# Optimization experiments

Hardware: AMD Instinct MI355X
Metric: run time of the kernel (lower is better)

## Reference

```python
import jax, jax.numpy as jnp
import numpy as np

NUM_HEADS = 4
C_IN = 80   # in_channels[0] (raw camera BEV channels)
C = 126     # in_channels[1]
D = C + 2   # 128, inner attention dim


def _conv(x, w, b=None):
    # NCHW conv, 3x3, SAME padding (padding=1)
    y = jax.lax.conv_general_dilated(x, w, (1, 1), 'SAME',
                                     dimension_numbers=('NCHW', 'OIHW', 'NCHW'))
    if b is not None:
        y = y + b[None, :, None, None]
    return y


def setup_inputs() -> dict:
    key = jax.random.key(0)
    ks = jax.random.split(key, 16)
    s = 0.02
    inp = {
        'lidar_bev': jax.random.normal(ks[0], (1, C, 64, 64), jnp.float32),
        'cam_bev': jax.random.normal(ks[1], (1, C_IN, 64, 64), jnp.float32),
        'cam_enc_w': jax.random.normal(ks[2], (C, C_IN, 3, 3), jnp.float32) * s,
        'cam_enc_b': jnp.zeros((C,), jnp.float32),
        'cam_v_w': jax.random.normal(ks[3], (D, C), jnp.float32) * s,
        'cam_qk_w': jax.random.normal(ks[4], (2 * D, C), jnp.float32) * s,
        'cam_proj_w': jax.random.normal(ks[5], (C, D), jnp.float32) * s,
        'cam_proj_b': jnp.zeros((C,), jnp.float32),
        'lidar_v_w': jax.random.normal(ks[6], (D, C), jnp.float32) * s,
        'lidar_qk_w': jax.random.normal(ks[7], (2 * D, C), jnp.float32) * s,
        'lidar_proj_w': jax.random.normal(ks[8], (C, D), jnp.float32) * s,
        'lidar_proj_b': jnp.zeros((C,), jnp.float32),
        'fuser_w': jax.random.normal(ks[9], (C, 4 * C, 3, 3), jnp.float32) * s,
    }
    return inp


def reference(lidar_bev, cam_bev, cam_enc_w, cam_enc_b, cam_v_w, cam_qk_w,
              cam_proj_w, cam_proj_b, lidar_v_w, lidar_qk_w, lidar_proj_w,
              lidar_proj_b, fuser_w):
    B, Cc, H, W = lidar_bev.shape
    N = H * W
    nh, hd = NUM_HEADS, D // NUM_HEADS
    scale = Cc ** (-0.5)  # in_channels[1] ** -0.5

    cam_enc = _conv(cam_bev, cam_enc_w, cam_enc_b)  # [B,C,H,W] (SCNET stand-in)

    cam_f = cam_enc.reshape(B, Cc, N).transpose(0, 2, 1)     # [B,N,C]
    lid_f = lidar_bev.reshape(B, Cc, N).transpose(0, 2, 1)    # [B,N,C]

    def heads(x):  # [B,N,D] -> [B,nh,N,hd]
        return x.reshape(B, N, nh, hd).transpose(0, 2, 1, 3)

    cam_v = heads(cam_f @ cam_v_w.T)
    lid_v = heads(lid_f @ lidar_v_w.T)

    def qk(x, w):  # -> (q, k) each [B,nh,N,hd]
        t = (x @ w.T).reshape(B, N, 2, nh, hd).transpose(2, 0, 3, 1, 4)
        return t[0], t[1]

    lid_q, lid_k = qk(lid_f, lidar_qk_w)
    cam_q, cam_k = qk(cam_f, cam_qk_w)

    def merge(o):  # [B,nh,N,hd] -> [B,N,D]
        return o.transpose(0, 2, 1, 3).reshape(B, N, D)

    def to_map(x):  # [B,N,C] -> [B,C,H,W]
        return x.reshape(B, H, W, Cc).transpose(0, 3, 1, 2)

    # lidar-driven attention, reused against two value tensors
    lid_attn = jax.nn.softmax(jnp.einsum('bhnd,bhmd->bhnm', lid_q, lid_k) * scale, axis=-1)
    cam_by_lid = to_map(merge(lid_attn @ cam_v) @ cam_proj_w.T + cam_proj_b)
    cam_bev_l = cam_enc + cam_by_lid
    lid_by_lid = to_map(merge(lid_attn @ lid_v) @ lidar_proj_w.T + lidar_proj_b)
    lidar_bev_l = lidar_bev + lid_by_lid

    # camera-driven attention (note: original code uses lidar_proj for BOTH outputs here)
    cam_attn = jax.nn.softmax(jnp.einsum('bhnd,bhmd->bhnm', cam_q, cam_k) * scale, axis=-1)
    cam_by_cam = to_map(merge(cam_attn @ cam_v) @ lidar_proj_w.T + lidar_proj_b)
    cam_bev_c = cam_enc + cam_by_cam
    lid_by_cam = to_map(merge(cam_attn @ lid_v) @ lidar_proj_w.T + lidar_proj_b)
    lidar_bev_c = lidar_bev + lid_by_cam

    fused_in = jnp.concatenate([cam_bev_c, cam_bev_l, lidar_bev_c, lidar_bev_l], axis=1)
    return _conv(fused_in, fuser_w)
```

## Files before the change

kernel.cpp:

```cpp
#include <hip/hip_runtime.h>
#include <hip/hip_bf16.h>

typedef unsigned short ushort_t;
using f32x4  = __attribute__((ext_vector_type(4))) float;
using f32x16 = __attribute__((ext_vector_type(16))) float;
using bf16x8 = __attribute__((ext_vector_type(8))) short;
typedef unsigned uint2v __attribute__((ext_vector_type(2)));

#define N_PIX 4096

static __device__ __forceinline__ unsigned short f2bf(float f) {
  unsigned int u = __builtin_bit_cast(unsigned int, f);
  u += 0x7FFFu + ((u >> 16) & 1u);
  return (unsigned short)(u >> 16);
}
static __device__ __forceinline__ float bf2f(unsigned int us) {
  return __builtin_bit_cast(float, us << 16);
}

typedef union {
  uint4 u4;
  unsigned u[4];
  unsigned long long q[2];
  bf16x8 v;
  unsigned short us[8];
} fragU;

#define LDS_U32(p) ((unsigned)(uintptr_t)((__attribute__((address_space(3))) void*)(p)))

__global__ __launch_bounds__(256) void zero_span_k(uint4* __restrict__ p, int n16) {
  int i = blockIdx.x * 256 + threadIdx.x;
  if (i < n16) p[i] = (uint4){0u, 0u, 0u, 0u};
}

__global__ __launch_bounds__(256) void pack_w_k(
    const float* __restrict__ cam_enc_w, const float* __restrict__ fuser_w,
    const float* __restrict__ lid_proj_w, const float* __restrict__ cam_proj_w,
    const float* __restrict__ lid_qk_w, const float* __restrict__ cam_qk_w,
    const float* __restrict__ cam_v_w, const float* __restrict__ lid_v_w,
    ushort_t* __restrict__ Wp_c, ushort_t* __restrict__ Wp_f,
    ushort_t* __restrict__ Wp_lid, ushort_t* __restrict__ Wp_cam,
    ushort_t* __restrict__ Wq) {
  const float QSCALE = 0.08908708063747479f * 1.4426950408889634f;
  int idx = blockIdx.x * 256 + threadIdx.x;
  if (idx < 110592) {
    int kk = idx / 12288, r = idx % 12288;
    int co = r / 96, ci = r % 96;
    float v = (co < 126 && ci < 80) ? cam_enc_w[(co * 80 + ci) * 9 + kk] : 0.f;
    Wp_c[idx] = f2bf(v);
  } else if (idx < 700416) {
    int j = idx - 110592;
    int kk = j / 65536, r = j % 65536;
    int co = r / 512, ci = r % 512;
    float v = (co < 126 && ci < 504) ? fuser_w[(co * 504 + ci) * 9 + kk] : 0.f;
    Wp_f[j] = f2bf(v);
  } else if (idx < 716800) {
    int j = idx - 700416;
    int co = j >> 7, k = j & 127;
    Wp_lid[j] = f2bf(co < 126 ? lid_proj_w[co * 128 + k] : 0.f);
  } else if (idx < 733184) {
    int j = idx - 716800;
    int co = j >> 7, k = j & 127;
    Wp_cam[j] = f2bf(co < 126 ? cam_proj_w[co * 128 + k] : 0.f);
  } else if (idx < 831488) {
    int j = idx - 733184;
    int t = j >> 14, r = j & 16383;
    int row = r >> 7, ci = r & 127;
    float v = 0.f;
    if (ci < 126) {
      if (t == 0)      v = lid_qk_w[row * 126 + ci] * QSCALE;
      else if (t == 1) v = lid_qk_w[(128 + row) * 126 + ci];
      else if (t == 2) v = cam_qk_w[row * 126 + ci] * QSCALE;
      else if (t == 3) v = cam_qk_w[(128 + row) * 126 + ci];
      else if (t == 4) v = cam_v_w[row * 126 + ci];
      else             v = lid_v_w[row * 126 + ci];
    }
    Wq[j] = f2bf(v);
  }
}

__global__ __launch_bounds__(256) void convert_in_k(
    const float* __restrict__ cam, const float* __restrict__ lidar,
    ushort_t* __restrict__ m, ushort_t* __restrict__ h,
    ushort_t* __restrict__ lidBF) {
  int idx = blockIdx.x * 256 + threadIdx.x;
  if (idx < 327680) {
    int ch = idx >> 12, n = idx & 4095;
    int y = n >> 6, x = n & 63;
    unsigned short b = f2bf(cam[idx]);
    m[ch * 4224 + (y + 1) * 64 + x] = b;
    h[ch * 4356 + (y + 1) * 66 + (x + 1)] = b;
  } else {
    int j = idx - 327680;
    if (j < 516096) lidBF[j] = f2bf(lidar[j]);
  }
}

__global__ __launch_bounds__(256) void conv_mfma_k(
    const ushort_t* __restrict__ Amain,
    const ushort_t* __restrict__ Ahalo,
    const ushort_t* __restrict__ Wp,
    ushort_t* __restrict__ parts,
    int CIp, int ksteps) {
  __shared__ __align__(16) ushort_t Abuf[2][2048];
  const int y   = blockIdx.x;
  const int kk  = blockIdx.y;
  const int ky  = kk / 3, kx = kk - ky * 3;
  const int tid = threadIdx.x;
  const int w   = tid >> 6, l = tid & 63;
  const int lane15 = l & 15, g = l >> 4;
  const int yy1 = y + ky;

  const int ci_l = w * 8 + (l >> 5) * 4 + ((l & 7) >> 1);
  const int m0   = ((l >> 3) & 3) * 16 + (l & 1) * 8;
  const ushort_t* src;
  size_t plane;
  if (kx == 1) { plane = 66 * 64; src = Amain + (size_t)ci_l * plane + yy1 * 64 + m0; }
  else         { plane = 66 * 66; src = Ahalo + (size_t)ci_l * plane + yy1 * 66 + m0 + kx; }

  const ushort_t* wbase = Wp + ((size_t)kk * 128 + w * 32 + lane15) * CIp + g * 8;
  const unsigned tr_base = LDS_U32(&Abuf[0][0]) + (unsigned)(g * 1024 + lane15 * 8);

  f32x4 acc[4][2];
  #pragma unroll
  for (int q = 0; q < 4; ++q) {
    acc[q][0] = (f32x4){0.f, 0.f, 0.f, 0.f};
    acc[q][1] = (f32x4){0.f, 0.f, 0.f, 0.f};
  }

  __builtin_amdgcn_global_load_lds(
      (const __attribute__((address_space(1))) unsigned*)src,
      (__attribute__((address_space(3))) unsigned*)(&Abuf[0][w * 512]), 16, 0, 0);
  __syncthreads();

  for (int s = 0; s < ksteps; ++s) {
    if (s + 1 < ksteps) {
      const ushort_t* srcn = src + (size_t)(s + 1) * 32 * plane;
      __builtin_amdgcn_global_load_lds(
          (const __attribute__((address_space(1))) unsigned*)srcn,
          (__attribute__((address_space(3))) unsigned*)(&Abuf[(s + 1) & 1][w * 512]), 16, 0, 0);
    }
    const ushort_t* wb = wbase + s * 32;
    fragU fb0, fb1;
    fb0.u4 = *(const uint4*)(wb);
    fb1.u4 = *(const uint4*)(wb + 16 * CIp);

    unsigned ta = tr_base + (unsigned)((s & 1) << 12);
    unsigned long long r00, r01, r10, r11, r20, r21, r30, r31;
    asm volatile("ds_read_b64_tr_b16 %0, %1 offset:0"   : "=v"(r00) : "v"(ta));
    asm volatile("ds_read_b64_tr_b16 %0, %1 offset:512" : "=v"(r01) : "v"(ta));
    asm volatile("ds_read_b64_tr_b16 %0, %1 offset:128" : "=v"(r10) : "v"(ta));
    asm volatile("ds_read_b64_tr_b16 %0, %1 offset:640" : "=v"(r11) : "v"(ta));
    asm volatile("ds_read_b64_tr_b16 %0, %1 offset:256" : "=v"(r20) : "v"(ta));
    asm volatile("ds_read_b64_tr_b16 %0, %1 offset:768" : "=v"(r21) : "v"(ta));
    asm volatile("ds_read_b64_tr_b16 %0, %1 offset:384" : "=v"(r30) : "v"(ta));
    asm volatile("ds_read_b64_tr_b16 %0, %1 offset:896" : "=v"(r31) : "v"(ta));
    asm volatile("s_waitcnt lgkmcnt(0)" ::: "memory");
    __builtin_amdgcn_sched_barrier(0);

    fragU fa;
    fa.q[0] = r00; fa.q[1] = r01;
    acc[0][0] = __builtin_amdgcn_mfma_f32_16x16x32_bf16(fa.v, fb0.v, acc[0][0], 0, 0, 0);
    acc[0][1] = __builtin_amdgcn_mfma_f32_16x16x32_bf16(fa.v, fb1.v, acc[0][1], 0, 0, 0);
    fa.q[0] = r10; fa.q[1] = r11;
    acc[1][0] = __builtin_amdgcn_mfma_f32_16x16x32_bf16(fa.v, fb0.v, acc[1][0], 0, 0, 0);
    acc[1][1] = __builtin_amdgcn_mfma_f32_16x16x32_bf16(fa.v, fb1.v, acc[1][1], 0, 0, 0);
    fa.q[0] = r20; fa.q[1] = r21;
    acc[2][0] = __builtin_amdgcn_mfma_f32_16x16x32_bf16(fa.v, fb0.v, acc[2][0], 0, 0, 0);
    acc[2][1] = __builtin_amdgcn_mfma_f32_16x16x32_bf16(fa.v, fb1.v, acc[2][1], 0, 0, 0);
    fa.q[0] = r30; fa.q[1] = r31;
    acc[3][0] = __builtin_amdgcn_mfma_f32_16x16x32_bf16(fa.v, fb0.v, acc[3][0], 0, 0, 0);
    acc[3][1] = __builtin_amdgcn_mfma_f32_16x16x32_bf16(fa.v, fb1.v, acc[3][1], 0, 0, 0);
    __syncthreads();
  }

  ushort_t* pout = parts + (size_t)kk * 524288 + (size_t)(w * 32 + lane15) * 4096
                 + y * 64 + g * 4;
  #pragma unroll
  for (int q = 0; q < 4; ++q) {
    ushort4 p0, p1;
    p0.x = f2bf(acc[q][0][0]); p0.y = f2bf(acc[q][0][1]);
    p0.z = f2bf(acc[q][0][2]); p0.w = f2bf(acc[q][0][3]);
    p1.x = f2bf(acc[q][1][0]); p1.y = f2bf(acc[q][1][1]);
    p1.z = f2bf(acc[q][1][2]); p1.w = f2bf(acc[q][1][3]);
    *(ushort4*)(pout + q * 16)             = p0;
    *(ushort4*)(pout + 16 * 4096 + q * 16) = p1;
  }
}

__global__ __launch_bounds__(256) void reduce9_k(
    const ushort_t* __restrict__ parts, float* __restrict__ out,
    ushort_t* __restrict__ outbf, const float* __restrict__ bias) {
  int n0 = (blockIdx.x * 256 + threadIdx.x) * 8;
  int co = blockIdx.y;
  size_t off = (size_t)co * 4096 + n0;
  float s[8] = {0, 0, 0, 0, 0, 0, 0, 0};
  #pragma unroll
  for (int kk = 0; kk < 9; ++kk) {
    uint4 v = *(const uint4*)(parts + (size_t)kk * 524288 + off);
    s[0] += bf2f(v.x & 0xffffu); s[1] += bf2f(v.x >> 16);
    s[2] += bf2f(v.y & 0xffffu); s[3] += bf2f(v.y >> 16);
    s[4] += bf2f(v.z & 0xffffu); s[5] += bf2f(v.z >> 16);
    s[6] += bf2f(v.w & 0xffffu); s[7] += bf2f(v.w >> 16);
  }
  float b = bias ? bias[co] : 0.f;
  #pragma unroll
  for (int i = 0; i < 8; ++i) s[i] += b;
  f32x4 o0 = {s[0], s[1], s[2], s[3]};
  f32x4 o1 = {s[4], s[5], s[6], s[7]};
  *(f32x4*)(out + off)     = o0;
  *(f32x4*)(out + off + 4) = o1;
  if (outbf) {
    ushort4 b0, b1;
    b0.x = f2bf(s[0]); b0.y = f2bf(s[1]); b0.z = f2bf(s[2]); b0.w = f2bf(s[3]);
    b1.x = f2bf(s[4]); b1.y = f2bf(s[5]); b1.z = f2bf(s[6]); b1.w = f2bf(s[7]);
    *(ushort4*)(outbf + off)     = b0;
    *(ushort4*)(outbf + off + 4) = b1;
  }
}

__global__ __launch_bounds__(256) void qkv_mfma_k(
    const ushort_t* __restrict__ lidBF, const ushort_t* __restrict__ camBF,
    const ushort_t* __restrict__ Wq,
    ushort_t* __restrict__ lidQK, ushort_t* __restrict__ camQK,
    ushort_t* __restrict__ camV, ushort_t* __restrict__ lidV) {
  __shared__ __align__(16) ushort_t Abuf[2][2048];
  const int y = blockIdx.x, t = blockIdx.y;
  const ushort_t* X = (t >= 2 && t <= 4) ? camBF : lidBF;
  const int tid = threadIdx.x;
  const int w = tid >> 6, l = tid & 63;
  const int lane15 = l & 15, g = l >> 4;
  const int ci_l = w * 8 + (l >> 5) * 4 + ((l & 7) >> 1);
  const int m0   = ((l >> 3) & 3) * 16 + (l & 1) * 8;
  const ushort_t* src = X + (size_t)ci_l * 4096 + y * 64 + m0;
  const ushort_t* wbase = Wq + (size_t)t * 16384 + (w * 32 + lane15) * 128 + g * 8;
  const unsigned tr_base = LDS_U32(&Abuf[0][0]) + (unsigned)(g * 1024 + lane15 * 8);

  f32x4 acc[4][2];
  #pragma unroll
  for (int q = 0; q < 4; ++q) {
    acc[q][0] = (f32x4){0.f, 0.f, 0.f, 0.f};
    acc[q][1] = (f32x4){0.f, 0.f, 0.f, 0.f};
  }

  __builtin_amdgcn_global_load_lds(
      (const __attribute__((address_space(1))) unsigned*)src,
      (__attribute__((address_space(3))) unsigned*)(&Abuf[0][w * 512]), 16, 0, 0);
  __syncthreads();

  for (int s = 0; s < 4; ++s) {
    if (s < 3) {
      const ushort_t* srcn = src + (size_t)(s + 1) * 32 * 4096;
      __builtin_amdgcn_global_load_lds(
          (const __attribute__((address_space(1))) unsigned*)srcn,
          (__attribute__((address_space(3))) unsigned*)(&Abuf[(s + 1) & 1][w * 512]), 16, 0, 0);
    }
    const ushort_t* wb = wbase + s * 32;
    fragU fb0, fb1;
    fb0.u4 = *(const uint4*)(wb);
    fb1.u4 = *(const uint4*)(wb + 16 * 128);

    unsigned ta = tr_base + (unsigned)((s & 1) << 12);
    unsigned long long r00, r01, r10, r11, r20, r21, r30, r31;
    asm volatile("ds_read_b64_tr_b16 %0, %1 offset:0"   : "=v"(r00) : "v"(ta));
    asm volatile("ds_read_b64_tr_b16 %0, %1 offset:512" : "=v"(r01) : "v"(ta));
    asm volatile("ds_read_b64_tr_b16 %0, %1 offset:128" : "=v"(r10) : "v"(ta));
    asm volatile("ds_read_b64_tr_b16 %0, %1 offset:640" : "=v"(r11) : "v"(ta));
    asm volatile("ds_read_b64_tr_b16 %0, %1 offset:256" : "=v"(r20) : "v"(ta));
    asm volatile("ds_read_b64_tr_b16 %0, %1 offset:768" : "=v"(r21) : "v"(ta));
    asm volatile("ds_read_b64_tr_b16 %0, %1 offset:384" : "=v"(r30) : "v"(ta));
    asm volatile("ds_read_b64_tr_b16 %0, %1 offset:896" : "=v"(r31) : "v"(ta));
    asm volatile("s_waitcnt lgkmcnt(0)" ::: "memory");
    __builtin_amdgcn_sched_barrier(0);

    fragU fa;
    fa.q[0] = r00; fa.q[1] = r01;
    acc[0][0] = __builtin_amdgcn_mfma_f32_16x16x32_bf16(fa.v, fb0.v, acc[0][0], 0, 0, 0);
    acc[0][1] = __builtin_amdgcn_mfma_f32_16x16x32_bf16(fa.v, fb1.v, acc[0][1], 0, 0, 0);
    fa.q[0] = r10; fa.q[1] = r11;
    acc[1][0] = __builtin_amdgcn_mfma_f32_16x16x32_bf16(fa.v, fb0.v, acc[1][0], 0, 0, 0);
    acc[1][1] = __builtin_amdgcn_mfma_f32_16x16x32_bf16(fa.v, fb1.v, acc[1][1], 0, 0, 0);
    fa.q[0] = r20; fa.q[1] = r21;
    acc[2][0] = __builtin_amdgcn_mfma_f32_16x16x32_bf16(fa.v, fb0.v, acc[2][0], 0, 0, 0);
    acc[2][1] = __builtin_amdgcn_mfma_f32_16x16x32_bf16(fa.v, fb1.v, acc[2][1], 0, 0, 0);
    fa.q[0] = r30; fa.q[1] = r31;
    acc[3][0] = __builtin_amdgcn_mfma_f32_16x16x32_bf16(fa.v, fb0.v, acc[3][0], 0, 0, 0);
    acc[3][1] = __builtin_amdgcn_mfma_f32_16x16x32_bf16(fa.v, fb1.v, acc[3][1], 0, 0, 0);
    __syncthreads();
  }

  if (t < 4) {
    ushort_t* dst = (t < 2) ? lidQK : camQK;
    const int colbase = (t & 1) * 128 + w * 32 + lane15;
    #pragma unroll
    for (int q = 0; q < 4; ++q)
      #pragma unroll
      for (int tt = 0; tt < 2; ++tt)
        #pragma unroll
        for (int r = 0; r < 4; ++r) {
          int n = y * 64 + q * 16 + g * 4 + r;
          dst[(size_t)n * 256 + colbase + tt * 16] = f2bf(acc[q][tt][r]);
        }
  } else {
    ushort_t* dst = (t == 4) ? camV : lidV;
    ushort_t* pout = dst + (size_t)(w * 32 + lane15) * 4096 + y * 64 + g * 4;
    #pragma unroll
    for (int q = 0; q < 4; ++q) {
      ushort4 p0, p1;
      p0.x = f2bf(acc[q][0][0]); p0.y = f2bf(acc[q][0][1]);
      p0.z = f2bf(acc[q][0][2]); p0.w = f2bf(acc[q][0][3]);
      p1.x = f2bf(acc[q][1][0]); p1.y = f2bf(acc[q][1][1]);
      p1.z = f2bf(acc[q][1][2]); p1.w = f2bf(acc[q][1][3]);
      *(ushort4*)(pout + q * 16)             = p0;
      *(ushort4*)(pout + 16 * 4096 + q * 16) = p1;
    }
  }
}

__global__ __launch_bounds__(256) void flash_attn_mfma(
    const ushort_t* __restrict__ lidQK, const ushort_t* __restrict__ camQK,
    const ushort_t* __restrict__ camV, const ushort_t* __restrict__ lidV,
    ushort_t* __restrict__ OP, float2* __restrict__ ML) {
  const int i0    = blockIdx.x * 128;
  const int h     = blockIdx.y;
  const int attn  = blockIdx.z >> 1;
  const int half  = blockIdx.z & 1;
  const int kbase = half * 2048;
  const ushort_t* QK = attn ? camQK : lidQK;

  __shared__ __align__(16) ushort_t Ks[2][64 * 40];
  __shared__ __align__(16) ushort_t Vt[2][64 * 72];

  const int tid = threadIdx.x;
  const int w = tid >> 6, l = tid & 63;
  const int q31 = l & 31, hi = l >> 5;
  const int q0w = i0 + w * 32;

  const int srow = tid >> 2, sc = tid & 3;
  const ushort_t* Kg = QK + (size_t)(kbase + srow) * 256 + 128 + h * 32 + sc * 8;
  const ushort_t* Vg = ((srow >> 5) ? lidV : camV)
                     + (size_t)(h * 32 + (srow & 31)) * N_PIX + kbase;

  fragU qf0, qf1;
  qf0.u4 = *(const uint4*)(QK + (size_t)(q0w + q31) * 256 + h * 32 + hi * 8);
  qf1.u4 = *(const uint4*)(QK + (size_t)(q0w + q31) * 256 + h * 32 + 16 + hi * 8);

  {
    uint4 k4 = *(const uint4*)Kg;
    uint4 va = *(const uint4*)(Vg + sc * 8);
    uint4 vb = *(const uint4*)(Vg + (sc + 4) * 8);
    *(uint4*)(&Ks[0][srow * 40 + sc * 8]) = k4;
    *(uint4*)(&Vt[0][srow * 72 + sc * 8]) = va;
    *(uint4*)(&Vt[0][srow * 72 + (sc + 4) * 8]) = vb;
  }
  __syncthreads();

  f32x16 Oc = (f32x16)0.f, Ol = (f32x16)0.f;
  float lrun = 0.f, mrun = -1e30f;

  for (int it = 0; it < 32; ++it) {
    const int cur = it & 1, nxt = cur ^ 1;
    const bool more = (it + 1) < 32;
    uint4 kn, van, vbn;
    if (more) {
      kn  = *(const uint4*)(Kg + (size_t)(it + 1) * 16384);
      van = *(const uint4*)(Vg + (it + 1) * 64 + sc * 8);
      vbn = *(const uint4*)(Vg + (it + 1) * 64 + (sc + 4) * 8);
    }

    const ushort_t* kb = &Ks[cur][0];
    fragU k00, k01, k10, k11;
    k00.u4 = *(const uint4*)(kb + q31 * 40 + hi * 8);
    k01.u4 = *(const uint4*)(kb + q31 * 40 + 16 + hi * 8);
    k10.u4 = *(const uint4*)(kb + (32 + q31) * 40 + hi * 8);
    k11.u4 = *(const uint4*)(kb + (32 + q31) * 40 + 16 + hi * 8);
    f32x16 S0, S1;
    __builtin_amdgcn_s_setprio(1);
    S0 = __builtin_amdgcn_mfma_f32_32x32x16_bf16(k00.v, qf0.v, (f32x16)0.f, 0, 0, 0);
    S0 = __builtin_amdgcn_mfma_f32_32x32x16_bf16(k01.v, qf1.v, S0, 0, 0, 0);
    S1 = __builtin_amdgcn_mfma_f32_32x32x16_bf16(k10.v, qf0.v, (f32x16)0.f, 0, 0, 0);
    S1 = __builtin_amdgcn_mfma_f32_32x32x16_bf16(k11.v, qf1.v, S1, 0, 0, 0);
    __builtin_amdgcn_s_setprio(0);

    float mx = S0[0];
    #pragma unroll
    for (int j = 1; j < 16; ++j) mx = fmaxf(mx, S0[j]);
    #pragma unroll
    for (int j = 0; j < 16; ++j) mx = fmaxf(mx, S1[j]);
    if (__any(mx > mrun + 6.f)) {
      float gm = mx;
      gm = fmaxf(gm, __shfl_xor(gm, 1));
      gm = fmaxf(gm, __shfl_xor(gm, 2));
      gm = fmaxf(gm, __shfl_xor(gm, 4));
      gm = fmaxf(gm, __shfl_xor(gm, 8));
      gm = fmaxf(gm, __shfl_xor(gm, 16));
      gm = fmaxf(gm, __shfl_xor(gm, 32));
      if (gm > mrun) {
        float corr = __builtin_amdgcn_exp2f(mrun - gm);
        Oc = Oc * corr;
        Ol = Ol * corr;
        lrun *= corr;
        mrun = gm;
      }
    }
    float ps = 0.f;
    #pragma unroll
    for (int j = 0; j < 16; ++j) {
      float p = __builtin_amdgcn_exp2f(S0[j] - mrun);
      S0[j] = p; ps += p;
    }
    #pragma unroll
    for (int j = 0; j < 16; ++j) {
      float p = __builtin_amdgcn_exp2f(S1[j] - mrun);
      S1[j] = p; ps += p;
    }
    ps += __shfl_xor(ps, 32);
    lrun += ps;

    fragU pa0, pa1, pa2, pa3;
    {
      unsigned a0, a1, b0, b1;
      asm("v_cvt_pk_bf16_f32 %0, %1, %2" : "=v"(a0) : "v"(S0[0]),  "v"(S0[1]));
      asm("v_cvt_pk_bf16_f32 %0, %1, %2" : "=v"(a1) : "v"(S0[2]),  "v"(S0[3]));
      asm("v_cvt_pk_bf16_f32 %0, %1, %2" : "=v"(b0) : "v"(S0[4]),  "v"(S0[5]));
      asm("v_cvt_pk_bf16_f32 %0, %1, %2" : "=v"(b1) : "v"(S0[6]),  "v"(S0[7]));
      uint2v r0 = __builtin_amdgcn_permlane32_swap(a0, b0, false, false);
      uint2v r1 = __builtin_amdgcn_permlane32_swap(a1, b1, false, false);
      pa0.u[0] = r0[0]; pa0.u[1] = r1[0]; pa0.u[2] = r0[1]; pa0.u[3] = r1[1];
      asm("v_cvt_pk_bf16_f32 %0, %1, %2" : "=v"(a0) : "v"(S0[8]),  "v"(S0[9]));
      asm("v_cvt_pk_bf16_f32 %0, %1, %2" : "=v"(a1) : "v"(S0[10]), "v"(S0[11]));
      asm("v_cvt_pk_bf16_f32 %0, %1, %2" : "=v"(b0) : "v"(S0[12]), "v"(S0[13]));
      asm("v_cvt_pk_bf16_f32 %0, %1, %2" : "=v"(b1) : "v"(S0[14]), "v"(S0[15]));
      r0 = __builtin_amdgcn_permlane32_swap(a0, b0, false, false);
      r1 = __builtin_amdgcn_permlane32_swap(a1, b1, false, false);
      pa1.u[0] = r0[0]; pa1.u[1] = r1[0]; pa1.u[2] = r0[1]; pa1.u[3] = r1[1];
      asm("v_cvt_pk_bf16_f32 %0, %1, %2" : "=v"(a0) : "v"(S1[0]),  "v"(S1[1]));
      asm("v_cvt_pk_bf16_f32 %0, %1, %2" : "=v"(a1) : "v"(S1[2]),  "v"(S1[3]));
      asm("v_cvt_pk_bf16_f32 %0, %1, %2" : "=v"(b0) : "v"(S1[4]),  "v"(S1[5]));
      asm("v_cvt_pk_bf16_f32 %0, %1, %2" : "=v"(b1) : "v"(S1[6]),  "v"(S1[7]));
      r0 = __builtin_amdgcn_permlane32_swap(a0, b0, false, false);
      r1 = __builtin_amdgcn_permlane32_swap(a1, b1, false, false);
      pa2.u[0] = r0[0]; pa2.u[1] = r1[0]; pa2.u[2] = r0[1]; pa2.u[3] = r1[1];
      asm("v_cvt_pk_bf16_f32 %0, %1, %2" : "=v"(a0) : "v"(S1[8]),  "v"(S1[9]));
      asm("v_cvt_pk_bf16_f32 %0, %1, %2" : "=v"(a1) : "v"(S1[10]), "v"(S1[11]));
      asm("v_cvt_pk_bf16_f32 %0, %1, %2" : "=v"(b0) : "v"(S1[12]), "v"(S1[13]));
      asm("v_cvt_pk_bf16_f32 %0, %1, %2" : "=v"(b1) : "v"(S1[14]), "v"(S1[15]));
      r0 = __builtin_amdgcn_permlane32_swap(a0, b0, false, false);
      r1 = __builtin_amdgcn_permlane32_swap(a1, b1, false, false);
      pa3.u[0] = r0[0]; pa3.u[1] = r1[0]; pa3.u[2] = r0[1]; pa3.u[3] = r1[1];
    }

    const ushort_t* vb = &Vt[cur][0];
    __builtin_amdgcn_s_setprio(1);
    {
      fragU vc, vl;
      vc.u4 = *(const uint4*)(vb + q31 * 72 + hi * 8);
      vl.u4 = *(const uint4*)(vb + (32 + q31) * 72 + hi * 8);
      Oc = __builtin_amdgcn_mfma_f32_32x32x16_bf16(pa0.v, vc.v, Oc, 0, 0, 0);
      Ol = __builtin_amdgcn_mfma_f32_32x32x16_bf16(pa0.v, vl.v, Ol, 0, 0, 0);
      vc.u4 = *(const uint4*)(vb + q31 * 72 + 16 + hi * 8);
      vl.u4 = *(const uint4*)(vb + (32 + q31) * 72 + 16 + hi * 8);
      Oc = __builtin_amdgcn_mfma_f32_32x32x16_bf16(pa1.v, vc.v, Oc, 0, 0, 0);
      Ol = __builtin_amdgcn_mfma_f32_32x32x16_bf16(pa1.v, vl.v, Ol, 0, 0, 0);
      vc.u4 = *(const uint4*)(vb + q31 * 72 + 32 + hi * 8);
      vl.u4 = *(const uint4*)(vb + (32 + q31) * 72 + 32 + hi * 8);
      Oc = __builtin_amdgcn_mfma_f32_32x32x16_bf16(pa2.v, vc.v, Oc, 0, 0, 0);
      Ol = __builtin_amdgcn_mfma_f32_32x32x16_bf16(pa2.v, vl.v, Ol, 0, 0, 0);
      vc.u4 = *(const uint4*)(vb + q31 * 72 + 48 + hi * 8);
      vl.u4 = *(const uint4*)(vb + (32 + q31) * 72 + 48 + hi * 8);
      Oc = __builtin_amdgcn_mfma_f32_32x32x16_bf16(pa3.v, vc.v, Oc, 0, 0, 0);
      Ol = __builtin_amdgcn_mfma_f32_32x32x16_bf16(pa3.v, vl.v, Ol, 0, 0, 0);
    }
    __builtin_amdgcn_s_setprio(0);

    if (more) {
      *(uint4*)(&Ks[nxt][srow * 40 + sc * 8]) = kn;
      *(uint4*)(&Vt[nxt][srow * 72 + sc * 8]) = van;
      *(uint4*)(&Vt[nxt][srow * 72 + (sc + 4) * 8]) = vbn;
    }
    __syncthreads();
  }

  ushort_t* OPc = OP + (size_t)((attn * 2 + half) * 2 + 0) * 4096 * 128;
  ushort_t* OPl = OP + (size_t)((attn * 2 + half) * 2 + 1) * 4096 * 128;
  const int d = h * 32 + q31;
  #pragma unroll
  for (int reg = 0; reg < 16; ++reg) {
    int n = q0w + (reg & 3) + 8 * (reg >> 2) + 4 * hi;
    OPc[(size_t)n * 128 + d] = f2bf(Oc[reg]);
    OPl[(size_t)n * 128 + d] = f2bf(Ol[reg]);
  }
  if (l < 32) {
    float2 v; v.x = mrun; v.y = lrun;
    ML[(size_t)(attn * 2 + half) * 4096 + q0w + l] = v;
  }
}

__global__ __launch_bounds__(256) void proj_mfma_k(
    const ushort_t* __restrict__ OP, const float2* __restrict__ ML,
    const ushort_t* __restrict__ Wlid, const ushort_t* __restrict__ Wcam,
    const float* __restrict__ cam_enc, const float* __restrict__ lidar_bev,
    const float* __restrict__ cam_proj_b, const float* __restrict__ lid_proj_b,
    ushort_t* __restrict__ fm, ushort_t* __restrict__ fh) {
  const int n0 = blockIdx.x * 64;
  const int ot = blockIdx.y;
  const int attn = (ot == 0 || ot == 2) ? 1 : 0;
  const int vt = ot >> 1;
  const int tid = threadIdx.x;
  const int w = tid >> 6, l = tid & 63;
  const int m = l & 15, g = l >> 4;

  const ushort_t* Oa = OP + (size_t)((attn * 2 + 0) * 2 + vt) * 4096 * 128;
  const ushort_t* Ob = OP + (size_t)((attn * 2 + 1) * 2 + vt) * 4096 * 128;
  const float2* MLa = ML + (size_t)(attn * 2 + 0) * 4096;
  const float2* MLb = ML + (size_t)(attn * 2 + 1) * 4096;

  const int arow = n0 + w * 16 + m;
  float2 mla = MLa[arow], mlb = MLb[arow];
  float M  = fmaxf(mla.x, mlb.x);
  float wa = __builtin_amdgcn_exp2f(mla.x - M);
  float wb = __builtin_amdgcn_exp2f(mlb.x - M);
  float dn = wa * mla.y + wb * mlb.y;
  float aa = wa / dn, ab = wb / dn;

  fragU afr[4];
  #pragma unroll
  for (int s = 0; s < 4; ++s) {
    fragU xa, xb;
    xa.u4 = *(const uint4*)(Oa + (size_t)arow * 128 + s * 32 + g * 8);
    xb.u4 = *(const uint4*)(Ob + (size_t)arow * 128 + s * 32 + g * 8);
    #pragma unroll
    for (int j = 0; j < 8; ++j)
      afr[s].us[j] = f2bf(aa * bf2f(xa.us[j]) + ab * bf2f(xb.us[j]));
  }

  const ushort_t* W = (ot == 1) ? Wcam : Wlid;
  f32x4 acc[8];
  #pragma unroll
  for (int t = 0; t < 8; ++t) acc[t] = (f32x4){0.f, 0.f, 0.f, 0.f};
  #pragma unroll
  for (int s = 0; s < 4; ++s) {
    #pragma unroll
    for (int t = 0; t < 8; ++t) {
      fragU bfr;
      bfr.u4 = *(const uint4*)(W + (size_t)(t * 16 + m) * 128 + s * 32 + g * 8);
      acc[t] = __builtin_amdgcn_mfma_f32_16x16x32_bf16(afr[s].v, bfr.v, acc[t], 0, 0, 0);
    }
  }

  const float* res  = (ot < 2) ? cam_enc : lidar_bev;
  const float* bias = (ot == 1) ? cam_proj_b : lid_proj_b;
  const int doff = ot * 126;
  #pragma unroll
  for (int t = 0; t < 8; ++t) {
    int co = t * 16 + m;
    if (co < 126) {
      float b = bias[co];
      #pragma unroll
      for (int r = 0; r < 4; ++r) {
        int n = n0 + w * 16 + g * 4 + r;
        float v = acc[t][r] + res[(size_t)co * N_PIX + n] + b;
        unsigned short bf = f2bf(v);
        int y = n >> 6, x = n & 63;
        fm[(doff + co) * 4224 + (y + 1) * 64 + x]      = bf;
        fh[(doff + co) * 4356 + (y + 1) * 66 + x + 1]  = bf;
      }
    }
  }
}

extern "C" void kernel_launch(void* const* d_in, const int* in_sizes, int n_in,
                              void* d_out, int out_size, void* d_ws, size_t ws_size,
                              hipStream_t stream) {
  (void)in_sizes; (void)n_in; (void)out_size; (void)ws_size;
  const float* lidar_bev  = (const float*)d_in[0];
  const float* cam_bev    = (const float*)d_in[1];
  const float* cam_enc_w  = (const float*)d_in[2];
  const float* cam_enc_b  = (const float*)d_in[3];
  const float* cam_v_w    = (const float*)d_in[4];
  const float* cam_qk_w   = (const float*)d_in[5];
  const float* cam_proj_w = (const float*)d_in[6];
  const float* cam_proj_b = (const float*)d_in[7];
  const float* lid_v_w    = (const float*)d_in[8];
  const float* lid_qk_w   = (const float*)d_in[9];
  const float* lid_proj_w = (const float*)d_in[10];
  const float* lid_proj_b = (const float*)d_in[11];
  const float* fuser_w    = (const float*)d_in[12];
  float* out = (float*)d_out;

  char* p = (char*)d_ws;
  ushort_t* arena = (ushort_t*)p;
  ushort_t* OP    = (ushort_t*)p;
  float2*   ML    = (float2*)(p + 8388608);
  ushort_t* lidQK = (ushort_t*)(p + 9437184);
  ushort_t* camQK = (ushort_t*)(p + 11534336);
  ushort_t* camV  = (ushort_t*)(p + 13631488);
  ushort_t* lidV  = (ushort_t*)(p + 14680064);
  float*    cam_enc = (float*)(p + 15728640);
  ushort_t* Wp_c    = (ushort_t*)(p + 17793024);
  ushort_t* Wp_f    = (ushort_t*)(p + 18014208);
  ushort_t* Wp_lid  = (ushort_t*)(p + 19193856);
  ushort_t* Wp_cam  = (ushort_t*)(p + 19226624);
  ushort_t* Wq      = (ushort_t*)(p + 19259392);
  ushort_t* lidBF   = (ushort_t*)(p + 19456000);
  ushort_t* camBF   = (ushort_t*)(p + 20504576);
  ushort_t* camBF_m = (ushort_t*)(p + 21553152);
  ushort_t* camBF_h = (ushort_t*)(p + 22364160);
  ushort_t* fusBF_m = (ushort_t*)(p + 23200512);
  ushort_t* fusBF_h = (ushort_t*)(p + 27525888);

  zero_span_k<<<2548, 256, 0, stream>>>((uint4*)(p + 21553152), 652080);
  pack_w_k<<<3248, 256, 0, stream>>>(cam_enc_w, fuser_w, lid_proj_w, cam_proj_w,
                                     lid_qk_w, cam_qk_w, cam_v_w, lid_v_w,
                                     Wp_c, Wp_f, Wp_lid, Wp_cam, Wq);
  convert_in_k<<<3296, 256, 0, stream>>>(cam_bev, lidar_bev, camBF_m, camBF_h, lidBF);

  conv_mfma_k<<<dim3(64, 9), 256, 0, stream>>>(camBF_m, camBF_h, Wp_c, arena, 96, 3);
  reduce9_k<<<dim3(2, 126), 256, 0, stream>>>(arena, cam_enc, camBF, cam_enc_b);

  qkv_mfma_k<<<dim3(64, 6), 256, 0, stream>>>(lidBF, camBF, Wq, lidQK, camQK, camV, lidV);
  flash_attn_mfma<<<dim3(32, 4, 4), 256, 0, stream>>>(lidQK, camQK, camV, lidV, OP, ML);
  proj_mfma_k<<<dim3(64, 4), 256, 0, stream>>>(OP, ML, Wp_lid, Wp_cam, cam_enc, lidar_bev,
                                               cam_proj_b, lid_proj_b, fusBF_m, fusBF_h);

  conv_mfma_k<<<dim3(64, 9), 256, 0, stream>>>(fusBF_m, fusBF_h, Wp_f, arena, 512, 16);
  reduce9_k<<<dim3(2, 126), 256, 0, stream>>>(arena, out, nullptr, nullptr);
}
```

Before: 117.2 us.

## Split flash attention keys three ways and drop fp32 cam_enc buffer

The attention kernel's key range is now split into three chunks per attention type instead of two, giving 6 z-slices and 768 workgroups instead of 512, which fills the GPU's compute units better. The projection kernel merges three partial softmax results instead of two. The fp32 cam_enc intermediate is no longer written; the residual is read from the bf16 copy instead. This cuts memory traffic but adds bf16 rounding to the residual, and the extra partial outputs are placed in reused workspace regions.

```diff
diff --git a/kernel.cpp b/kernel.cpp
--- a/kernel.cpp
+++ b/kernel.cpp
@@ -27,6 +27,14 @@
 } fragU;
 
 #define LDS_U32(p) ((unsigned)(uintptr_t)((__attribute__((address_space(3))) void*)(p)))
+
+static __device__ __forceinline__ size_t op_off(int s) {
+  return (s < 9) ? ((size_t)s << 20)
+       : (s == 9)  ? (size_t)15728640u
+       : (s == 10) ? (size_t)19456000u
+       :             (size_t)21553152u;
+}
+#define ML_OFF 16777216u
 
 __global__ __launch_bounds__(256) void zero_span_k(uint4* __restrict__ p, int n16) {
   int i = blockIdx.x * 256 + threadIdx.x;
@@ -206,10 +214,12 @@
   float b = bias ? bias[co] : 0.f;
   #pragma unroll
   for (int i = 0; i < 8; ++i) s[i] += b;
-  f32x4 o0 = {s[0], s[1], s[2], s[3]};
-  f32x4 o1 = {s[4], s[5], s[6], s[7]};
-  *(f32x4*)(out + off)     = o0;
-  *(f32x4*)(out + off + 4) = o1;
+  if (out) {
+    f32x4 o0 = {s[0], s[1], s[2], s[3]};
+    f32x4 o1 = {s[4], s[5], s[6], s[7]};
+    *(f32x4*)(out + off)     = o0;
+    *(f32x4*)(out + off + 4) = o1;
+  }
   if (outbf) {
     ushort4 b0, b1;
     b0.x = f2bf(s[0]); b0.y = f2bf(s[1]); b0.z = f2bf(s[2]); b0.w = f2bf(s[3]);
@@ -320,12 +330,14 @@
 __global__ __launch_bounds__(256) void flash_attn_mfma(
     const ushort_t* __restrict__ lidQK, const ushort_t* __restrict__ camQK,
     const ushort_t* __restrict__ camV, const ushort_t* __restrict__ lidV,
-    ushort_t* __restrict__ OP, float2* __restrict__ ML) {
+    char* __restrict__ ws) {
   const int i0    = blockIdx.x * 128;
   const int h     = blockIdx.y;
-  const int attn  = blockIdx.z >> 1;
-  const int half  = blockIdx.z & 1;
-  const int kbase = half * 2048;
+  const int z     = blockIdx.z;
+  const int attn  = (z >= 3) ? 1 : 0;
+  const int third = z - attn * 3;
+  const int kbase = (third == 0) ? 0 : (1408 + (third - 1) * 1344);
+  const int iters = (third == 0) ? 22 : 21;
   const ushort_t* QK = attn ? camQK : lidQK;
 
   __shared__ __align__(16) ushort_t Ks[2][64 * 40];
@@ -358,9 +370,9 @@
   f32x16 Oc = (f32x16)0.f, Ol = (f32x16)0.f;
   float lrun = 0.f, mrun = -1e30f;
 
-  for (int it = 0; it < 32; ++it) {
+  for (int it = 0; it < iters; ++it) {
     const int cur = it & 1, nxt = cur ^ 1;
-    const bool more = (it + 1) < 32;
+    const bool more = (it + 1) < iters;
     uint4 kn, van, vbn;
     if (more) {
       kn  = *(const uint4*)(Kg + (size_t)(it + 1) * 16384);
@@ -481,8 +493,10 @@
     __syncthreads();
   }
 
-  ushort_t* OPc = OP + (size_t)((attn * 2 + half) * 2 + 0) * 4096 * 128;
-  ushort_t* OPl = OP + (size_t)((attn * 2 + half) * 2 + 1) * 4096 * 128;
+  const int si = (attn * 3 + third) * 2;
+  ushort_t* OPc = (ushort_t*)(ws + op_off(si + 0));
+  ushort_t* OPl = (ushort_t*)(ws + op_off(si + 1));
+  float2* ML = (float2*)(ws + ML_OFF);
   const int d = h * 32 + q31;
   #pragma unroll
   for (int reg = 0; reg < 16; ++reg) {
@@ -492,14 +506,14 @@
   }
   if (l < 32) {
     float2 v; v.x = mrun; v.y = lrun;
-    ML[(size_t)(attn * 2 + half) * 4096 + q0w + l] = v;
+    ML[(size_t)(attn * 3 + third) * 4096 + q0w + l] = v;
   }
 }
 
 __global__ __launch_bounds__(256) void proj_mfma_k(
-    const ushort_t* __restrict__ OP, const float2* __restrict__ ML,
+    const char* __restrict__ ws,
     const ushort_t* __restrict__ Wlid, const ushort_t* __restrict__ Wcam,
-    const float* __restrict__ cam_enc, const float* __restrict__ lidar_bev,
+    const ushort_t* __restrict__ camBF, const float* __restrict__ lidar_bev,
     const float* __restrict__ cam_proj_b, const float* __restrict__ lid_proj_b,
     ushort_t* __restrict__ fm, ushort_t* __restrict__ fh) {
   const int n0 = blockIdx.x * 64;
@@ -510,28 +524,34 @@
   const int w = tid >> 6, l = tid & 63;
   const int m = l & 15, g = l >> 4;
 
-  const ushort_t* Oa = OP + (size_t)((attn * 2 + 0) * 2 + vt) * 4096 * 128;
-  const ushort_t* Ob = OP + (size_t)((attn * 2 + 1) * 2 + vt) * 4096 * 128;
-  const float2* MLa = ML + (size_t)(attn * 2 + 0) * 4096;
-  const float2* MLb = ML + (size_t)(attn * 2 + 1) * 4096;
-
+  const float2* ML = (const float2*)(ws + ML_OFF);
   const int arow = n0 + w * 16 + m;
-  float2 mla = MLa[arow], mlb = MLb[arow];
-  float M  = fmaxf(mla.x, mlb.x);
-  float wa = __builtin_amdgcn_exp2f(mla.x - M);
-  float wb = __builtin_amdgcn_exp2f(mlb.x - M);
-  float dn = wa * mla.y + wb * mlb.y;
-  float aa = wa / dn, ab = wb / dn;
+
+  float2 ml0 = ML[(size_t)(attn * 3 + 0) * 4096 + arow];
+  float2 ml1 = ML[(size_t)(attn * 3 + 1) * 4096 + arow];
+  float2 ml2 = ML[(size_t)(attn * 3 + 2) * 4096 + arow];
+  float M = fmaxf(fmaxf(ml0.x, ml1.x), ml2.x);
+  float w0 = __builtin_amdgcn_exp2f(ml0.x - M);
+  float w1 = __builtin_amdgcn_exp2f(ml1.x - M);
+  float w2 = __builtin_amdgcn_exp2f(ml2.x - M);
+  float dn = w0 * ml0.y + w1 * ml1.y + w2 * ml2.y;
+  float a0 = w0 / dn, a1 = w1 / dn, a2 = w2 / dn;
+
+  const ushort_t* O0 = (const ushort_t*)(ws + op_off((attn * 3 + 0) * 2 + vt));
+  const ushort_t* O1 = (const ushort_t*)(ws + op_off((attn * 3 + 1) * 2 + vt));
+  const ushort_t* O2 = (const ushort_t*)(ws + op_off((attn * 3 + 2) * 2 + vt));
 
   fragU afr[4];
   #pragma unroll
   for (int s = 0; s < 4; ++s) {
-    fragU xa, xb;
-    xa.u4 = *(const uint4*)(Oa + (size_t)arow * 128 + s * 32 + g * 8);
-    xb.u4 = *(const uint4*)(Ob + (size_t)arow * 128 + s * 32 + g * 8);
+    fragU x0, x1, x2;
+    x0.u4 = *(const uint4*)(O0 + (size_t)arow * 128 + s * 32 + g * 8);
+    x1.u4 = *(const uint4*)(O1 + (size_t)arow * 128 + s * 32 + g * 8);
+    x2.u4 = *(const uint4*)(O2 + (size_t)arow * 128 + s * 32 + g * 8);
     #pragma unroll
     for (int j = 0; j < 8; ++j)
-      afr[s].us[j] = f2bf(aa * bf2f(xa.us[j]) + ab * bf2f(xb.us[j]));
+      afr[s].us[j] = f2bf(a0 * bf2f(x0.us[j]) + a1 * bf2f(x1.us[j])
+                        + a2 * bf2f(x2.us[j]));
   }
 
   const ushort_t* W = (ot == 1) ? Wcam : Wlid;
@@ -548,7 +568,6 @@
     }
   }
 
-  const float* res  = (ot < 2) ? cam_enc : lidar_bev;
   const float* bias = (ot == 1) ? cam_proj_b : lid_proj_b;
   const int doff = ot * 126;
   #pragma unroll
@@ -559,7 +578,9 @@
       #pragma unroll
       for (int r = 0; r < 4; ++r) {
         int n = n0 + w * 16 + g * 4 + r;
-        float v = acc[t][r] + res[(size_t)co * N_PIX + n] + b;
+        float res = (ot < 2) ? bf2f(camBF[(size_t)co * N_PIX + n])
+                             : lidar_bev[(size_t)co * N_PIX + n];
+        float v = acc[t][r] + res + b;
         unsigned short bf = f2bf(v);
         int y = n >> 6, x = n & 63;
         fm[(doff + co) * 4224 + (y + 1) * 64 + x]      = bf;
@@ -590,13 +611,10 @@
 
   char* p = (char*)d_ws;
   ushort_t* arena = (ushort_t*)p;
-  ushort_t* OP    = (ushort_t*)p;
-  float2*   ML    = (float2*)(p + 8388608);
   ushort_t* lidQK = (ushort_t*)(p + 9437184);
   ushort_t* camQK = (ushort_t*)(p + 11534336);
   ushort_t* camV  = (ushort_t*)(p + 13631488);
   ushort_t* lidV  = (ushort_t*)(p + 14680064);
-  float*    cam_enc = (float*)(p + 15728640);
   ushort_t* Wp_c    = (ushort_t*)(p + 17793024);
   ushort_t* Wp_f    = (ushort_t*)(p + 18014208);
   ushort_t* Wp_lid  = (ushort_t*)(p + 19193856);
@@ -616,11 +634,11 @@
   convert_in_k<<<3296, 256, 0, stream>>>(cam_bev, lidar_bev, camBF_m, camBF_h, lidBF);
 
   conv_mfma_k<<<dim3(64, 9), 256, 0, stream>>>(camBF_m, camBF_h, Wp_c, arena, 96, 3);
-  reduce9_k<<<dim3(2, 126), 256, 0, stream>>>(arena, cam_enc, camBF, cam_enc_b);
+  reduce9_k<<<dim3(2, 126), 256, 0, stream>>>(arena, nullptr, camBF, cam_enc_b);
 
   qkv_mfma_k<<<dim3(64, 6), 256, 0, stream>>>(lidBF, camBF, Wq, lidQK, camQK, camV, lidV);
-  flash_attn_mfma<<<dim3(32, 4, 4), 256, 0, stream>>>(lidQK, camQK, camV, lidV, OP, ML);
-  proj_mfma_k<<<dim3(64, 4), 256, 0, stream>>>(OP, ML, Wp_lid, Wp_cam, cam_enc, lidar_bev,
+  flash_attn_mfma<<<dim3(32, 4, 6), 256, 0, stream>>>(lidQK, camQK, camV, lidV, p);
+  proj_mfma_k<<<dim3(64, 4), 256, 0, stream>>>(p, Wp_lid, Wp_cam, camBF, lidar_bev,
                                                cam_proj_b, lid_proj_b, fusBF_m, fusBF_h);
 
   conv_mfma_k<<<dim3(64, 9), 256, 0, stream>>>(fusBF_m, fusBF_h, Wp_f, arena, 512, 16);
```

After: 119.8 us. 2.2% more time.
